# Kernel optimization log

Hardware: AMD Instinct MI355X
Metric: run time of the kernel (lower is better)

Reference implementation:

```python
import jax, jax.numpy as jnp
import numpy as np

EPS = 1e-05

def setup_inputs() -> dict:
    key = jax.random.key(0)
    k1, k2, k3 = jax.random.split(key, 3)
    B, S, D_IN, D_OUT = 4, 2048, 4096, 12288
    x = jax.random.normal(k1, (B, S, D_IN), dtype=jnp.float32)
    weight = jax.random.normal(k2, (D_OUT, D_IN), dtype=jnp.float32) * (1.0 / np.sqrt(D_IN))
    bias = jnp.zeros((D_OUT,), dtype=jnp.float32)
    ln_weight = jnp.ones((D_IN,), dtype=jnp.float32)
    ln_bias = jnp.zeros((D_IN,), dtype=jnp.float32)
    return {"x": x, "weight": weight, "bias": bias, "ln_weight": ln_weight, "ln_bias": ln_bias}

def reference(x, weight, bias, ln_weight, ln_bias):
    # LayerNorm over last dim
    mean = jnp.mean(x, axis=-1, keepdims=True)
    var = jnp.mean(jnp.square(x - mean), axis=-1, keepdims=True)
    normed = (x - mean) * jax.lax.rsqrt(var + EPS) * ln_weight + ln_bias
    # Linear: y = normed @ W^T + b
    return jnp.einsum('bsd,od->bso', normed, weight) + bias
```

## Files before the change

kernel.cpp:

```cpp
#include <hip/hip_runtime.h>
#include <hip/hip_bf16.h>
#include <stdint.h>

typedef __attribute__((ext_vector_type(8))) short short8_t;
typedef __attribute__((ext_vector_type(4))) float f32x4;

__device__ __forceinline__ unsigned short f2bf(float f) {
  union { float f; unsigned int u; } a;
  a.f = f;
  unsigned int u = a.u;
  u += 0x7fffu + ((u >> 16) & 1u);
  return (unsigned short)(u >> 16);
}

__device__ __forceinline__ void gload_lds16(const void* g, void* l) {
  __builtin_amdgcn_global_load_lds(
      (const __attribute__((address_space(1))) void*)g,
      (__attribute__((address_space(3))) void*)l, 16, 0, 0);
}

constexpr int D_IN = 4096;

__global__ __launch_bounds__(256) void ln_bf16_kernel(
    const float* __restrict__ x, const float* __restrict__ lnw,
    const float* __restrict__ lnb, unsigned short* __restrict__ out) {
  const int row = blockIdx.x;
  const int tid = threadIdx.x;
  const float* xr = x + (size_t)row * D_IN;

  f32x4 v[4];
  float sum = 0.f, sq = 0.f;
#pragma unroll
  for (int i = 0; i < 4; ++i) {
    v[i] = __builtin_nontemporal_load(
        reinterpret_cast<const f32x4*>(xr + i * 1024 + tid * 4));
    sum += v[i][0] + v[i][1] + v[i][2] + v[i][3];
    sq += v[i][0]*v[i][0] + v[i][1]*v[i][1] + v[i][2]*v[i][2] + v[i][3]*v[i][3];
  }
#pragma unroll
  for (int off = 32; off > 0; off >>= 1) {
    sum += __shfl_down(sum, off, 64);
    sq  += __shfl_down(sq, off, 64);
  }
  __shared__ float s_sum[4], s_sq[4];
  if ((tid & 63) == 0) { s_sum[tid >> 6] = sum; s_sq[tid >> 6] = sq; }
  __syncthreads();
  const float fs = s_sum[0] + s_sum[1] + s_sum[2] + s_sum[3];
  const float fq = s_sq[0] + s_sq[1] + s_sq[2] + s_sq[3];
  const float mean = fs * (1.f / D_IN);
  const float var = fq * (1.f / D_IN) - mean * mean;
  const float rstd = rsqrtf(var + 1e-5f);

  unsigned short* orow = out + (size_t)row * D_IN;
#pragma unroll
  for (int i = 0; i < 4; ++i) {
    const int col = i * 1024 + tid * 4;
    const f32x4 w = *reinterpret_cast<const f32x4*>(lnw + col);
    const f32x4 b = *reinterpret_cast<const f32x4*>(lnb + col);
    ushort4 o;
    o.x = f2bf((v[i][0] - mean) * rstd * w[0] + b[0]);
    o.y = f2bf((v[i][1] - mean) * rstd * w[1] + b[1]);
    o.z = f2bf((v[i][2] - mean) * rstd * w[2] + b[2]);
    o.w = f2bf((v[i][3] - mean) * rstd * w[3] + b[3]);
    *reinterpret_cast<ushort4*>(orow + col) = o;
  }
}

__global__ __launch_bounds__(256) void f32_to_bf16_kernel(
    const float* __restrict__ in, unsigned short* __restrict__ out) {
  const size_t i = ((size_t)blockIdx.x * 256 + threadIdx.x) * 8;
  const f32x4 a = __builtin_nontemporal_load(reinterpret_cast<const f32x4*>(in + i));
  const f32x4 b = __builtin_nontemporal_load(reinterpret_cast<const f32x4*>(in + i + 4));
  ushort4 lo, hi;
  lo.x = f2bf(a[0]); lo.y = f2bf(a[1]); lo.z = f2bf(a[2]); lo.w = f2bf(a[3]);
  hi.x = f2bf(b[0]); hi.y = f2bf(b[1]); hi.z = f2bf(b[2]); hi.w = f2bf(b[3]);
  *reinterpret_cast<ushort4*>(out + i) = lo;
  *reinterpret_cast<ushort4*>(out + i + 4) = hi;
}


#define RD(P, IMM) (*reinterpret_cast<const short8_t*>((P) + (IMM)))

#define READ6(S, KK)                                                \
  _Pragma("unroll") for (int m_ = 0; m_ < 4; ++m_)                  \
    af[m_] = RD((KK) ? aB1 : aB0, (S)*16384 + m_*2048);             \
  _Pragma("unroll") for (int n_ = 0; n_ < 2; ++n_)                  \
    bfr[n_] = RD((KK) ? bB1 : bB0, (S)*16384 + n_*2048);

#define MFMA8                                                       \
  _Pragma("unroll") for (int m_ = 0; m_ < 4; ++m_) {                \
    _Pragma("unroll") for (int n_ = 0; n_ < 2; ++n_)                \
      acc[m_][n_] = __builtin_amdgcn_mfma_f32_16x16x32_bf16(        \
          af[m_], bfr[n_], acc[m_][n_], 0, 0, 0);                   \
  }

#define STAGE_A(S, U, KT) \
  gload_lds16(aSrc + (size_t)((U)*64) * K + (size_t)(KT)*64, ldsAw + (S)*16384 + (U)*8192)
#define STAGE_B(S, U, KT) \
  gload_lds16(bSrc + (size_t)((U)*64) * K + (size_t)(KT)*64, ldsBw + (S)*16384 + (U)*8192)
#define STAGE_ALL(S, KT)                                            \
  STAGE_A(S,0,KT); STAGE_A(S,1,KT); STAGE_B(S,0,KT); STAGE_B(S,1,KT);

#define XREG(S)                                                     \
  READ6(S, 0)                                                       \
  __builtin_amdgcn_s_setprio(1);                                    \
  MFMA8                                                             \
  READ6(S, 1)                                                       \
  __builtin_amdgcn_s_setprio(0);                                    \
  asm volatile("s_waitcnt lgkmcnt(0)" ::: "memory");                \
  __builtin_amdgcn_s_barrier();                                     \
  asm volatile("" ::: "memory");

#define YREG(S, KT)                                                 \
  STAGE_ALL(S, KT)                                                  \
  __builtin_amdgcn_s_setprio(1);                                    \
  MFMA8                                                             \
  __builtin_amdgcn_s_setprio(0);                                    \
  asm volatile("s_waitcnt vmcnt(4)" ::: "memory");                  \
  __builtin_amdgcn_s_barrier();                                     \
  asm volatile("" ::: "memory");

__global__ __launch_bounds__(512, 4) void gemm_xy128(
    const unsigned short* __restrict__ A,
    const unsigned short* __restrict__ B,
    const float* __restrict__ bias,
    float* __restrict__ C,
    int M, int N, int K, int NYB, int BXP) {
  extern __shared__ char smem[];
  const int tid = threadIdx.x;
  const int lane = tid & 63;
  const int wid = tid >> 6;
  const int wr = wid >> 2, wc = wid & 3;
  const int fr = lane & 15;
  const int q16 = (lane >> 4) * 16;

  const int id = blockIdx.x;
  const int xcd = id & 7;
  const int s = id >> 3;
  const int gsz = 8 * BXP;
  const int g = s / gsz;
  const int j = s - g * gsz;
  const int by = g * 8 + (j & 7);
  const int bx = xcd * BXP + (j >> 3);
  const int m0 = by * 128, n0 = bx * 128;

  const int s_log = (tid * 16) ^ (((tid >> 3) & 7) << 4);
  const int rsw = s_log >> 7;
  const int csw = (s_log & 127) >> 1;
  const unsigned short* aSrc = A + (size_t)(m0 + rsw) * K + csw;
  const unsigned short* bSrc = B + (size_t)(n0 + rsw) * K + csw;

  char* const ldsAw = smem + wid * 1024;
  char* const ldsBw = smem + 32768 + wid * 1024;

  const int s7 = (fr & 7) << 4;
  const char* const aB0 = smem + (wr * 64 + fr) * 128 + (q16 ^ s7);
  const char* const aB1 = smem + (wr * 64 + fr) * 128 + ((64 + q16) ^ s7);
  const char* const bB0 = smem + 32768 + (wc * 32 + fr) * 128 + (q16 ^ s7);
  const char* const bB1 = smem + 32768 + (wc * 32 + fr) * 128 + ((64 + q16) ^ s7);

  f32x4 acc[4][2] = {};
  short8_t af[4], bfr[2];

  STAGE_ALL(0, 0)
  STAGE_ALL(1, 1)
  asm volatile("s_waitcnt vmcnt(4)" ::: "memory");
  __builtin_amdgcn_s_barrier();
  asm volatile("" ::: "memory");

  const int NK = K >> 6;
  for (int t = 0; t < (NK - 2) >> 1; ++t) {
    XREG(0) YREG(0, 2*t + 2)
    XREG(1) YREG(1, 2*t + 3)
  }
  {
    READ6(0, 0)
    __builtin_amdgcn_s_setprio(1);
    MFMA8
    READ6(0, 1)
    MFMA8
    __builtin_amdgcn_s_setprio(0);
    asm volatile("s_waitcnt lgkmcnt(0)\n\ts_waitcnt vmcnt(0)" ::: "memory");
    __builtin_amdgcn_s_barrier();
    asm volatile("" ::: "memory");
    READ6(1, 0)
    __builtin_amdgcn_s_setprio(1);
    MFMA8
    READ6(1, 1)
    MFMA8
    __builtin_amdgcn_s_setprio(0);
  }

  const int fq = lane >> 4;
  float bv[2];
#pragma unroll
  for (int n = 0; n < 2; ++n) bv[n] = bias[n0 + wc * 32 + n * 16 + fr];
#pragma unroll
  for (int m = 0; m < 4; ++m) {
#pragma unroll
    for (int jj = 0; jj < 4; ++jj) {
      const int row = m0 + wr * 64 + m * 16 + fq * 4 + jj;
      float* Crow = C + (size_t)row * N + n0 + wc * 32 + fr;
#pragma unroll
      for (int n = 0; n < 2; ++n)
        __builtin_nontemporal_store(acc[m][n][jj] + bv[n], Crow + n * 16);
    }
  }
}

extern "C" void kernel_launch(void* const* d_in, const int* in_sizes, int n_in,
                              void* d_out, int out_size, void* d_ws, size_t ws_size,
                              hipStream_t stream) {
  const float* x    = (const float*)d_in[0];
  const float* w    = (const float*)d_in[1];
  const float* bias = (const float*)d_in[2];
  const float* lnw  = (const float*)d_in[3];
  const float* lnb  = (const float*)d_in[4];
  float* out = (float*)d_out;

  const int DIN  = 4096;
  const int M    = in_sizes[0] / DIN;
  const int DOUT = in_sizes[2];

  unsigned short* normA = (unsigned short*)d_ws;
  unsigned short* wB    = normA + (size_t)M * DIN;

  ln_bf16_kernel<<<M, 256, 0, stream>>>(x, lnw, lnb, normA);
  f32_to_bf16_kernel<<<((size_t)DOUT * DIN) / (256 * 8), 256, 0, stream>>>(w, wB);

  const int nwg = (M / 128) * (DOUT / 128);
  (void)hipFuncSetAttribute((const void*)gemm_xy128,
                            hipFuncAttributeMaxDynamicSharedMemorySize, 65536);
  gemm_xy128<<<nwg, 512, 65536, stream>>>(normA, wB, bias, out,
                                          M, DOUT, DIN, M / 128, (DOUT / 128) / 8);
}
```

Measured before the change: 813.4 us.

## Enlarge GEMM tile to 256x256 and load B fragments directly from global into registers

```diff
diff --git a/kernel.cpp b/kernel.cpp
--- a/kernel.cpp
+++ b/kernel.cpp
@@ -81,46 +81,49 @@
 
 #define RD(P, IMM) (*reinterpret_cast<const short8_t*>((P) + (IMM)))
 
-#define READ6(S, KK)                                                \
-  _Pragma("unroll") for (int m_ = 0; m_ < 4; ++m_)                  \
-    af[m_] = RD((KK) ? aB1 : aB0, (S)*16384 + m_*2048);             \
-  _Pragma("unroll") for (int n_ = 0; n_ < 2; ++n_)                  \
-    bfr[n_] = RD((KK) ? bB1 : bB0, (S)*16384 + n_*2048);
-
-#define MFMA8                                                       \
-  _Pragma("unroll") for (int m_ = 0; m_ < 4; ++m_) {                \
-    _Pragma("unroll") for (int n_ = 0; n_ < 2; ++n_)                \
+#define READ_A8(S, KK)                                              \
+  _Pragma("unroll") for (int m_ = 0; m_ < 8; ++m_)                  \
+    af[m_] = RD((KK) ? aB1 : aB0, (S)*32768 + m_*2048);
+
+#define LOADB(BF, KT, KK)                                           \
+  _Pragma("unroll") for (int n_ = 0; n_ < 4; ++n_)                  \
+    BF[n_] = *reinterpret_cast<const short8_t*>(                    \
+        bG + (size_t)n_ * 16 * K + (KT)*64 + (KK)*32);
+
+#define MFMA32(BF)                                                  \
+  _Pragma("unroll") for (int m_ = 0; m_ < 8; ++m_) {                \
+    _Pragma("unroll") for (int n_ = 0; n_ < 4; ++n_)                \
       acc[m_][n_] = __builtin_amdgcn_mfma_f32_16x16x32_bf16(        \
-          af[m_], bfr[n_], acc[m_][n_], 0, 0, 0);                   \
-  }
-
-#define STAGE_A(S, U, KT) \
-  gload_lds16(aSrc + (size_t)((U)*64) * K + (size_t)(KT)*64, ldsAw + (S)*16384 + (U)*8192)
-#define STAGE_B(S, U, KT) \
-  gload_lds16(bSrc + (size_t)((U)*64) * K + (size_t)(KT)*64, ldsBw + (S)*16384 + (U)*8192)
-#define STAGE_ALL(S, KT)                                            \
-  STAGE_A(S,0,KT); STAGE_A(S,1,KT); STAGE_B(S,0,KT); STAGE_B(S,1,KT);
-
-#define XREG(S)                                                     \
-  READ6(S, 0)                                                       \
+          af[m_], BF[n_], acc[m_][n_], 0, 0, 0);                    \
+  }
+
+#define STAGE_A4(S, KT)                                             \
+  gload_lds16(aSrc + (size_t)(KT)*64,                 ldsAw + (S)*32768);          \
+  gload_lds16(aSrc + (size_t)64*K  + (size_t)(KT)*64, ldsAw + (S)*32768 + 8192);   \
+  gload_lds16(aSrc + (size_t)128*K + (size_t)(KT)*64, ldsAw + (S)*32768 + 16384);  \
+  gload_lds16(aSrc + (size_t)192*K + (size_t)(KT)*64, ldsAw + (S)*32768 + 24576);
+
+#define XREG(S, KT)                                                 \
+  LOADB(bfB, KT, 1)                                                 \
+  READ_A8(S, 0)                                                     \
   __builtin_amdgcn_s_setprio(1);                                    \
-  MFMA8                                                             \
-  READ6(S, 1)                                                       \
+  MFMA32(bfA)                                                       \
   __builtin_amdgcn_s_setprio(0);                                    \
+  READ_A8(S, 1)                                                     \
   asm volatile("s_waitcnt lgkmcnt(0)" ::: "memory");                \
   __builtin_amdgcn_s_barrier();                                     \
   asm volatile("" ::: "memory");
 
-#define YREG(S, KT)                                                 \
-  STAGE_ALL(S, KT)                                                  \
+#define YREG(S, KT2, KTB)                                           \
+  STAGE_A4(S, KT2)                                                  \
+  LOADB(bfA, KTB, 0)                                                \
   __builtin_amdgcn_s_setprio(1);                                    \
-  MFMA8                                                             \
+  MFMA32(bfB)                                                       \
   __builtin_amdgcn_s_setprio(0);                                    \
-  asm volatile("s_waitcnt vmcnt(4)" ::: "memory");                  \
   __builtin_amdgcn_s_barrier();                                     \
   asm volatile("" ::: "memory");
 
-__global__ __launch_bounds__(512, 4) void gemm_xy128(
+__global__ __launch_bounds__(512, 2) void gemm_bdir(
     const unsigned short* __restrict__ A,
     const unsigned short* __restrict__ B,
     const float* __restrict__ bias,
@@ -142,67 +145,64 @@
   const int j = s - g * gsz;
   const int by = g * 8 + (j & 7);
   const int bx = xcd * BXP + (j >> 3);
-  const int m0 = by * 128, n0 = bx * 128;
+  const int m0 = by * 256, n0 = bx * 256;
 
   const int s_log = (tid * 16) ^ (((tid >> 3) & 7) << 4);
   const int rsw = s_log >> 7;
   const int csw = (s_log & 127) >> 1;
   const unsigned short* aSrc = A + (size_t)(m0 + rsw) * K + csw;
-  const unsigned short* bSrc = B + (size_t)(n0 + rsw) * K + csw;
+
+  const unsigned short* bG = B + (size_t)(n0 + wc * 64 + fr) * K + (q16 >> 1);
 
   char* const ldsAw = smem + wid * 1024;
-  char* const ldsBw = smem + 32768 + wid * 1024;
 
   const int s7 = (fr & 7) << 4;
-  const char* const aB0 = smem + (wr * 64 + fr) * 128 + (q16 ^ s7);
-  const char* const aB1 = smem + (wr * 64 + fr) * 128 + ((64 + q16) ^ s7);
-  const char* const bB0 = smem + 32768 + (wc * 32 + fr) * 128 + (q16 ^ s7);
-  const char* const bB1 = smem + 32768 + (wc * 32 + fr) * 128 + ((64 + q16) ^ s7);
-
-  f32x4 acc[4][2] = {};
-  short8_t af[4], bfr[2];
-
-  STAGE_ALL(0, 0)
-  STAGE_ALL(1, 1)
-  asm volatile("s_waitcnt vmcnt(4)" ::: "memory");
+  const char* const aB0 = smem + (wr * 128 + fr) * 128 + (q16 ^ s7);
+  const char* const aB1 = smem + (wr * 128 + fr) * 128 + ((64 + q16) ^ s7);
+
+  f32x4 acc[8][4] = {};
+  short8_t af[8];
+  short8_t bfA[4], bfB[4];
+
+  STAGE_A4(0, 0)
+  STAGE_A4(1, 1)
+  LOADB(bfA, 0, 0)
+  asm volatile("s_waitcnt vmcnt(8)" ::: "memory");
   __builtin_amdgcn_s_barrier();
   asm volatile("" ::: "memory");
 
   const int NK = K >> 6;
   for (int t = 0; t < (NK - 2) >> 1; ++t) {
-    XREG(0) YREG(0, 2*t + 2)
-    XREG(1) YREG(1, 2*t + 3)
+    const int k0 = 2*t, k1 = 2*t + 1;
+    XREG(0, k0)  YREG(0, k0 + 2, k1)
+    XREG(1, k1)  YREG(1, k1 + 2, k1 + 1)
   }
   {
-    READ6(0, 0)
+    XREG(0, NK - 2)
+    LOADB(bfA, NK - 1, 0)
     __builtin_amdgcn_s_setprio(1);
-    MFMA8
-    READ6(0, 1)
-    MFMA8
+    MFMA32(bfB)
     __builtin_amdgcn_s_setprio(0);
-    asm volatile("s_waitcnt lgkmcnt(0)\n\ts_waitcnt vmcnt(0)" ::: "memory");
     __builtin_amdgcn_s_barrier();
     asm volatile("" ::: "memory");
-    READ6(1, 0)
+    XREG(1, NK - 1)
     __builtin_amdgcn_s_setprio(1);
-    MFMA8
-    READ6(1, 1)
-    MFMA8
+    MFMA32(bfB)
     __builtin_amdgcn_s_setprio(0);
   }
 
   const int fq = lane >> 4;
-  float bv[2];
-#pragma unroll
-  for (int n = 0; n < 2; ++n) bv[n] = bias[n0 + wc * 32 + n * 16 + fr];
-#pragma unroll
-  for (int m = 0; m < 4; ++m) {
+  float bv[4];
+#pragma unroll
+  for (int n = 0; n < 4; ++n) bv[n] = bias[n0 + wc * 64 + n * 16 + fr];
+#pragma unroll
+  for (int m = 0; m < 8; ++m) {
 #pragma unroll
     for (int jj = 0; jj < 4; ++jj) {
-      const int row = m0 + wr * 64 + m * 16 + fq * 4 + jj;
-      float* Crow = C + (size_t)row * N + n0 + wc * 32 + fr;
-#pragma unroll
-      for (int n = 0; n < 2; ++n)
+      const int row = m0 + wr * 128 + m * 16 + fq * 4 + jj;
+      float* Crow = C + (size_t)row * N + n0 + wc * 64 + fr;
+#pragma unroll
+      for (int n = 0; n < 4; ++n)
         __builtin_nontemporal_store(acc[m][n][jj] + bv[n], Crow + n * 16);
     }
   }
@@ -228,9 +228,9 @@
   ln_bf16_kernel<<<M, 256, 0, stream>>>(x, lnw, lnb, normA);
   f32_to_bf16_kernel<<<((size_t)DOUT * DIN) / (256 * 8), 256, 0, stream>>>(w, wB);
 
-  const int nwg = (M / 128) * (DOUT / 128);
-  (void)hipFuncSetAttribute((const void*)gemm_xy128,
+  const int nwg = (M / 256) * (DOUT / 256);
+  (void)hipFuncSetAttribute((const void*)gemm_bdir,
                             hipFuncAttributeMaxDynamicSharedMemorySize, 65536);
-  gemm_xy128<<<nwg, 512, 65536, stream>>>(normA, wB, bias, out,
-                                          M, DOUT, DIN, M / 128, (DOUT / 128) / 8);
-}
+  gemm_bdir<<<nwg, 512, 65536, stream>>>(normA, wB, bias, out,
+                                         M, DOUT, DIN, M / 256, (DOUT / 256) / 8);
+}
```

Measured after the change: 1.144 ms. +40.7%, slower.
